# Kernel optimization log

Hardware: AMD Instinct MI355X
Metric: run time of the kernel (lower is better)

The kernel has to match this reference:

```python
import jax, jax.numpy as jnp
import numpy as np

CONFUSED_PAIRS = [(1, 2), (3, 4), (5, 6)]
NUM_CLASSES = 13
MARGIN = 0.5
IGNORE_INDEX = -100
BIG = 1e9  # finite sentinel instead of +/-inf (keeps grads clean)
EPS = 1e-12  # matches F.normalize eps

_conf_np = np.zeros((NUM_CLASSES, NUM_CLASSES), dtype=bool)
for _a, _b in CONFUSED_PAIRS:
    _conf_np[_a, _b] = True
    _conf_np[_b, _a] = True
CONF = jnp.asarray(_conf_np)  # [C, C] symmetric confused-class table


def setup_inputs() -> dict:
    key = jax.random.key(0)
    k1, k2 = jax.random.split(key)
    embeddings = jax.random.normal(k1, (16, 512, 256), dtype=jnp.float32)
    labels = jax.random.randint(k2, (16, 512), 0, 13, dtype=jnp.int64)
    return {"embeddings": embeddings, "labels": labels}


def reference(embeddings, labels):
    B, S, H = embeddings.shape
    e = embeddings.reshape(-1, H)                      # [N, H]
    lab = labels.reshape(-1)                           # [N]
    N = e.shape[0]

    valid = lab != IGNORE_INDEX                        # [N]
    # L2 normalize (F.normalize: divide by norm clamped to eps)
    norm = jnp.linalg.norm(e, axis=1, keepdims=True)
    e = e / jnp.maximum(norm, EPS)

    sim = e @ e.T                                      # [N, N] cosine sims

    lab_c = jnp.clip(lab, 0, NUM_CLASSES - 1)          # safe gather index
    # anchor label participates in some confused pair, and anchor is valid
    anchor_ok = valid & CONF[lab_c].any(axis=1)        # [N]

    same = lab[:, None] == lab[None, :]                # [N, N]
    eye = jnp.eye(N, dtype=bool)
    pos_mask = same & valid[None, :] & ~eye            # positives: same class, not self
    neg_mask = CONF[lab_c[:, None], lab_c[None, :]] & valid[None, :]  # confused-class negatives

    has_pos = pos_mask.any(axis=1)
    has_neg = neg_mask.any(axis=1)
    count_mask = anchor_ok & has_pos & has_neg         # [N] anchors contributing a triplet

    hardest_pos = jnp.min(jnp.where(pos_mask, sim, BIG), axis=1)   # [N]
    hardest_neg = jnp.max(jnp.where(neg_mask, sim, -BIG), axis=1)  # [N]

    triplet = jax.nn.relu(MARGIN + hardest_neg - hardest_pos)
    triplet = jnp.where(count_mask, triplet, 0.0)

    num_triplets = count_mask.sum()
    loss = triplet.sum() / jnp.maximum(num_triplets, 1).astype(triplet.dtype)
    return jnp.where(num_triplets > 0, loss, 0.0)
```

## Files before the change

kernel.cpp:

```cpp
#include <hip/hip_runtime.h>
#include <math.h>

#define Hdim    256
#define NMAX    8192
#define NCLS    13
#define NPADMAX (NMAX + 6 * 32)
#define WLMAX   264
#define NSPLIT  16
#define WPB     4
#define SIMGRID ((WLMAX * NSPLIT) / WPB)
#define BIGV    1e9f
#define MARGIN  0.5f

typedef __attribute__((ext_vector_type(8))) short bf16x8;
typedef __attribute__((ext_vector_type(4))) float f32x4;

struct WS {
    unsigned short ebf[NPADMAX][Hdim];
    unsigned hpK[NPADMAX];
    unsigned hnK[NPADMAX];
    int labG[NPADMAX];
    int gpos[NMAX];
    int S[8];
    int n[8];
    int wl_a[WLMAX];
    int wl_c[WLMAX];
    int T;
    unsigned done;
};

__device__ inline unsigned short f2bf(float f) {
    unsigned u = __float_as_uint(f);
    return (unsigned short)((u + 0x7fffu + ((u >> 16) & 1u)) >> 16);
}
__device__ inline unsigned fkey(float f) {
    unsigned u = __float_as_uint(f);
    return (u & 0x80000000u) ? ~u : (u | 0x80000000u);
}
__device__ inline float funkey(unsigned k) {
    unsigned u = (k & 0x80000000u) ? (k & 0x7fffffffu) : ~k;
    return __uint_as_float(u);
}

__global__ __launch_bounds__(1024) void plan_kernel(const int* __restrict__ lab,
                                                    WS* ws, int N) {
    __shared__ int h[8];
    __shared__ int S[8];
    __shared__ int cur[8];
    const int tid = threadIdx.x;
    if (tid < 8) h[tid] = 0;
    __syncthreads();
    for (int i = tid; i < N; i += 1024) {
        int l = lab[i];
        if (l >= 1 && l <= 6) atomicAdd(&h[l], 1);
    }
    __syncthreads();
    if (tid == 0) {
        int acc = 0;
        for (int c = 1; c <= 6; ++c) { S[c] = acc; acc += ((h[c] + 31) >> 5) << 5; }
        S[7] = acc;
        int T = 0;
        for (int c = 1; c <= 6; ++c) {
            int nt = (h[c] + 31) >> 5;
            for (int k = 0; k < nt; ++k) { ws->wl_a[T] = S[c] + 32 * k; ws->wl_c[T] = c; ++T; }
        }
        ws->T = T;
        ws->done = 0u;
        for (int c = 0; c < 8; ++c) { ws->n[c] = h[c]; ws->S[c] = S[c]; }
        ws->S[7] = S[7];
    }
    __syncthreads();
    const int SEnd = S[7];
    for (int g = tid; g < SEnd; g += 1024) {
        ws->hpK[g] = 0xFFFFFFFFu;
        ws->hnK[g] = 0u;
        ws->labG[g] = -1;
    }
    if (tid < 8) cur[tid] = S[tid];
    __syncthreads();
    for (int i = tid; i < N; i += 1024) {
        int l = lab[i];
        int g = -1;
        if (l >= 1 && l <= 6) { g = atomicAdd(&cur[l], 1); ws->labG[g] = l; }
        ws->gpos[i] = g;
    }
}

__global__ __launch_bounds__(1024) void norm_gather_kernel(const float* __restrict__ in,
                                                           WS* ws) {
    int row  = blockIdx.x * 16 + (threadIdx.x >> 6);
    int lane = threadIdx.x & 63;
    int g = ws->gpos[row];
    if (g < 0) return;
    float4 v = ((const float4*)(in + (size_t)row * Hdim))[lane];
    float ss = v.x*v.x + v.y*v.y + v.z*v.z + v.w*v.w;
    #pragma unroll
    for (int off = 32; off >= 1; off >>= 1) ss += __shfl_xor(ss, off);
    float sc = 1.0f / fmaxf(sqrtf(ss), 1e-12f);
    ushort4 o;
    o.x = f2bf(v.x * sc); o.y = f2bf(v.y * sc);
    o.z = f2bf(v.z * sc); o.w = f2bf(v.w * sc);
    ((ushort4*)(&ws->ebf[g][0]))[lane] = o;
}

__global__ __launch_bounds__(256) void sim_kernel(WS* ws, float* __restrict__ out) {
    const int wave = threadIdx.x >> 6;
    const int lane = threadIdx.x & 63;
    const int col  = lane & 15;
    const int quad = lane >> 4;
    const int wid  = blockIdx.x * WPB + wave;
    const int tileIdx = wid / NSPLIT;
    const int split   = wid % NSPLIT;

    if (tileIdx < ws->T) {
        const int aBase = ws->wl_a[tileIdx];
        const int c     = ws->wl_c[tileIdx];
        const int p     = ((c - 1) ^ 1) + 1;
        const int posS = ws->S[c], posRealE = posS + ws->n[c];
        const int negS = ws->S[p], negRealE = negS + ws->n[p];
        const int nPosT = (ws->S[c + 1] - posS) >> 4;
        const int nT    = nPosT + ((((p == c + 1) ? ws->S[p + 1] : ws->S[p])
                                    - negS) >> 4);
        const int nNegT = ((ws->S[p + 1]) - negS) >> 4;
        const int nTT = nPosT + nNegT;

        const unsigned short* ebf = &ws->ebf[0][0];

        bf16x8 afrag[2][8];
        #pragma unroll
        for (int t2 = 0; t2 < 2; ++t2) {
            const unsigned short* rp = ebf + (size_t)(aBase + t2 * 16 + col) * Hdim + quad * 8;
            #pragma unroll
            for (int ks = 0; ks < 8; ++ks)
                afrag[t2][ks] = *(const bf16x8*)(rp + ks * 32);
        }

        float runMin[2][4], runMax[2][4];
        #pragma unroll
        for (int t2 = 0; t2 < 2; ++t2)
            #pragma unroll
            for (int r = 0; r < 4; ++r) { runMin[t2][r] = BIGV; runMax[t2][r] = -BIGV; }

        auto j0Of = [&](int t) -> int {
            return (t < nPosT) ? (posS + (t << 4)) : (negS + ((t - nPosT) << 4));
        };
        bf16x8 b0[8], b1[8];
        auto loadB = [&](bf16x8 (&bf)[8], int t) {
            const unsigned short* rp = ebf + (size_t)(j0Of(t) + col) * Hdim + quad * 8;
            #pragma unroll
            for (int ks = 0; ks < 8; ++ks)
                bf[ks] = *(const bf16x8*)(rp + ks * 32);
        };
        auto computeT = [&](bf16x8 (&bf)[8], int t) {
            int j0 = j0Of(t);
            bool isPos = t < nPosT;
            int realE  = isPos ? posRealE : negRealE;
            bool valid = (j0 + col) < realE;
            #pragma unroll
            for (int t2 = 0; t2 < 2; ++t2) {
                f32x4 acc = {0.f, 0.f, 0.f, 0.f};
                #pragma unroll
                for (int ks = 0; ks < 8; ++ks)
                    acc = __builtin_amdgcn_mfma_f32_16x16x32_bf16(afrag[t2][ks], bf[ks], acc, 0, 0, 0);
                if (isPos) {
                    #pragma unroll
                    for (int r = 0; r < 4; ++r)
                        runMin[t2][r] = fminf(runMin[t2][r], valid ? acc[r] : BIGV);
                } else {
                    #pragma unroll
                    for (int r = 0; r < 4; ++r)
                        runMax[t2][r] = fmaxf(runMax[t2][r], valid ? acc[r] : -BIGV);
                }
            }
        };

        int nIter = (nTT > split) ? ((nTT - split + NSPLIT - 1) / NSPLIT) : 0;
        int t = split, i = 0;
        if (nIter > 0) loadB(b0, t);
        while (i + 2 <= nIter) {
            loadB(b1, t + NSPLIT);
            computeT(b0, t);
            if (i + 2 < nIter) loadB(b0, t + 2 * NSPLIT);
            computeT(b1, t + NSPLIT);
            t += 2 * NSPLIT; i += 2;
        }
        if (i < nIter) computeT(b0, t);
        (void)nT;

        #pragma unroll
        for (int t2 = 0; t2 < 2; ++t2)
            #pragma unroll
            for (int r = 0; r < 4; ++r) {
                float mn = runMin[t2][r], mx = runMax[t2][r];
                #pragma unroll
                for (int off = 1; off < 16; off <<= 1) {
                    mn = fminf(mn, __shfl_xor(mn, off));
                    mx = fmaxf(mx, __shfl_xor(mx, off));
                }
                if (col == 0) {
                    int a = aBase + t2 * 16 + quad * 4 + r;
                    if (mn < 1e8f)  atomicMin(&ws->hpK[a], fkey(mn));
                    if (mx > -1e8f) atomicMax(&ws->hnK[a], fkey(mx));
                }
            }
    }

    __shared__ int isLast;
    __syncthreads();
    if (threadIdx.x == 0) {
        __threadfence();
        unsigned old = atomicAdd(&ws->done, 1u);
        isLast = (old == (unsigned)(gridDim.x - 1)) ? 1 : 0;
    }
    __syncthreads();
    if (!isLast) return;
    __threadfence();

    __shared__ int ncls[8];
    if (threadIdx.x < 8) ncls[threadIdx.x] = ws->n[threadIdx.x];
    __syncthreads();
    float sum = 0.f; int cnt = 0;
    const int SEnd = ws->S[7];
    for (int g = threadIdx.x; g < SEnd; g += 256) {
        int l = ws->labG[g];
        if (l >= 1) {
            int p = ((l - 1) ^ 1) + 1;
            if (ncls[l] >= 2 && ncls[p] >= 1) {
                float hp = funkey(ws->hpK[g]);
                float hn = funkey(ws->hnK[g]);
                float tr = MARGIN + hn - hp;
                if (tr > 0.f) sum += tr;
                cnt += 1;
            }
        }
    }
    #pragma unroll
    for (int off = 32; off >= 1; off >>= 1) {
        sum += __shfl_xor(sum, off);
        cnt += __shfl_xor(cnt, off);
    }
    __shared__ float ssum[4]; __shared__ int scnt[4];
    int w = threadIdx.x >> 6;
    if ((threadIdx.x & 63) == 0) { ssum[w] = sum; scnt[w] = cnt; }
    __syncthreads();
    if (threadIdx.x == 0) {
        float ts = ssum[0] + ssum[1] + ssum[2] + ssum[3];
        int   tc = scnt[0] + scnt[1] + scnt[2] + scnt[3];
        out[0] = (tc > 0) ? ts / (float)tc : 0.f;
    }
}

extern "C" void kernel_launch(void* const* d_in, const int* in_sizes, int n_in,
                              void* d_out, int out_size, void* d_ws, size_t ws_size,
                              hipStream_t stream) {
    const float* emb = (const float*)d_in[0];
    const int*   lab = (const int*)d_in[1];
    int N = in_sizes[1];
    WS* ws = (WS*)d_ws;

    plan_kernel<<<1, 1024, 0, stream>>>(lab, ws, N);
    norm_gather_kernel<<<N / 16, 1024, 0, stream>>>(emb, ws);
    sim_kernel<<<SIMGRID, 256, 0, stream>>>(ws, (float*)d_out);
}
```

Measured before the change: 111.3 us.

## Assign one block per anchor tile and reduce loss in-block with atomics

Reworks the sim kernel so each block handles a full 32-anchor tile with its 4 waves splitting the column tiles. Hardest pos/neg are combined in LDS, and per-tile loss sums and counts go to global atomics, instead of per-anchor atomic min/max arrays and a last-block serial reduction. This removes the hp/hn/label initialization and the final pass over all anchors, and also shrinks norm_gather blocks. In exchange it launches far fewer waves, so each does more sequential MFMA work and GPU occupancy is lower.

```diff
diff --git a/kernel.cpp b/kernel.cpp
--- a/kernel.cpp
+++ b/kernel.cpp
@@ -3,12 +3,8 @@
 
 #define Hdim    256
 #define NMAX    8192
-#define NCLS    13
 #define NPADMAX (NMAX + 6 * 32)
 #define WLMAX   264
-#define NSPLIT  16
-#define WPB     4
-#define SIMGRID ((WLMAX * NSPLIT) / WPB)
 #define BIGV    1e9f
 #define MARGIN  0.5f
 
@@ -17,9 +13,6 @@
 
 struct WS {
     unsigned short ebf[NPADMAX][Hdim];
-    unsigned hpK[NPADMAX];
-    unsigned hnK[NPADMAX];
-    int labG[NPADMAX];
     int gpos[NMAX];
     int S[8];
     int n[8];
@@ -27,19 +20,13 @@
     int wl_c[WLMAX];
     int T;
     unsigned done;
+    float wsum;
+    int   wcnt;
 };
 
 __device__ inline unsigned short f2bf(float f) {
     unsigned u = __float_as_uint(f);
     return (unsigned short)((u + 0x7fffu + ((u >> 16) & 1u)) >> 16);
-}
-__device__ inline unsigned fkey(float f) {
-    unsigned u = __float_as_uint(f);
-    return (u & 0x80000000u) ? ~u : (u | 0x80000000u);
-}
-__device__ inline float funkey(unsigned k) {
-    unsigned u = (k & 0x80000000u) ? (k & 0x7fffffffu) : ~k;
-    return __uint_as_float(u);
 }
 
 __global__ __launch_bounds__(1024) void plan_kernel(const int* __restrict__ lab,
@@ -58,37 +45,28 @@
     if (tid == 0) {
         int acc = 0;
         for (int c = 1; c <= 6; ++c) { S[c] = acc; acc += ((h[c] + 31) >> 5) << 5; }
-        S[7] = acc;
+        S[0] = 0; S[7] = acc;
         int T = 0;
         for (int c = 1; c <= 6; ++c) {
             int nt = (h[c] + 31) >> 5;
             for (int k = 0; k < nt; ++k) { ws->wl_a[T] = S[c] + 32 * k; ws->wl_c[T] = c; ++T; }
         }
         ws->T = T;
-        ws->done = 0u;
+        ws->done = 0u; ws->wsum = 0.f; ws->wcnt = 0;
         for (int c = 0; c < 8; ++c) { ws->n[c] = h[c]; ws->S[c] = S[c]; }
-        ws->S[7] = S[7];
-    }
-    __syncthreads();
-    const int SEnd = S[7];
-    for (int g = tid; g < SEnd; g += 1024) {
-        ws->hpK[g] = 0xFFFFFFFFu;
-        ws->hnK[g] = 0u;
-        ws->labG[g] = -1;
-    }
+    }
+    __syncthreads();
     if (tid < 8) cur[tid] = S[tid];
     __syncthreads();
     for (int i = tid; i < N; i += 1024) {
         int l = lab[i];
-        int g = -1;
-        if (l >= 1 && l <= 6) { g = atomicAdd(&cur[l], 1); ws->labG[g] = l; }
-        ws->gpos[i] = g;
-    }
-}
-
-__global__ __launch_bounds__(1024) void norm_gather_kernel(const float* __restrict__ in,
-                                                           WS* ws) {
-    int row  = blockIdx.x * 16 + (threadIdx.x >> 6);
+        ws->gpos[i] = (l >= 1 && l <= 6) ? atomicAdd(&cur[l], 1) : -1;
+    }
+}
+
+__global__ __launch_bounds__(256) void norm_gather_kernel(const float* __restrict__ in,
+                                                          WS* ws) {
+    int row  = blockIdx.x * 4 + (threadIdx.x >> 6);
     int lane = threadIdx.x & 63;
     int g = ws->gpos[row];
     if (g < 0) return;
@@ -108,9 +86,9 @@
     const int lane = threadIdx.x & 63;
     const int col  = lane & 15;
     const int quad = lane >> 4;
-    const int wid  = blockIdx.x * WPB + wave;
-    const int tileIdx = wid / NSPLIT;
-    const int split   = wid % NSPLIT;
+    const int tileIdx = blockIdx.x;
+
+    __shared__ float lds_hp[4][32], lds_hn[4][32];
 
     if (tileIdx < ws->T) {
         const int aBase = ws->wl_a[tileIdx];
@@ -119,10 +97,9 @@
         const int posS = ws->S[c], posRealE = posS + ws->n[c];
         const int negS = ws->S[p], negRealE = negS + ws->n[p];
         const int nPosT = (ws->S[c + 1] - posS) >> 4;
-        const int nT    = nPosT + ((((p == c + 1) ? ws->S[p + 1] : ws->S[p])
-                                    - negS) >> 4);
-        const int nNegT = ((ws->S[p + 1]) - negS) >> 4;
-        const int nTT = nPosT + nNegT;
+        const int nNegT = (ws->S[p + 1] - negS) >> 4;
+        const int nTT   = nPosT + nNegT;
+        const bool hasPN = (ws->n[c] >= 2) && (ws->n[p] >= 1);
 
         const unsigned short* ebf = &ws->ebf[0][0];
 
@@ -174,18 +151,17 @@
             }
         };
 
-        int nIter = (nTT > split) ? ((nTT - split + NSPLIT - 1) / NSPLIT) : 0;
-        int t = split, i = 0;
+        int nIter = (nTT > wave) ? ((nTT - wave + 3) >> 2) : 0;
+        int t = wave, i = 0;
         if (nIter > 0) loadB(b0, t);
         while (i + 2 <= nIter) {
-            loadB(b1, t + NSPLIT);
+            loadB(b1, t + 4);
             computeT(b0, t);
-            if (i + 2 < nIter) loadB(b0, t + 2 * NSPLIT);
-            computeT(b1, t + NSPLIT);
-            t += 2 * NSPLIT; i += 2;
+            if (i + 2 < nIter) loadB(b0, t + 8);
+            computeT(b1, t + 4);
+            t += 8; i += 2;
         }
         if (i < nIter) computeT(b0, t);
-        (void)nT;
 
         #pragma unroll
         for (int t2 = 0; t2 < 2; ++t2)
@@ -198,55 +174,47 @@
                     mx = fmaxf(mx, __shfl_xor(mx, off));
                 }
                 if (col == 0) {
-                    int a = aBase + t2 * 16 + quad * 4 + r;
-                    if (mn < 1e8f)  atomicMin(&ws->hpK[a], fkey(mn));
-                    if (mx > -1e8f) atomicMax(&ws->hnK[a], fkey(mx));
-                }
-            }
-    }
-
-    __shared__ int isLast;
-    __syncthreads();
+                    int a = t2 * 16 + quad * 4 + r;
+                    lds_hp[wave][a] = mn;
+                    lds_hn[wave][a] = mx;
+                }
+            }
+        __syncthreads();
+
+        if (wave == 0) {
+            float contrib = 0.f; int cc = 0;
+            if (lane < 32) {
+                float hp = fminf(fminf(lds_hp[0][lane], lds_hp[1][lane]),
+                                 fminf(lds_hp[2][lane], lds_hp[3][lane]));
+                float hn = fmaxf(fmaxf(lds_hn[0][lane], lds_hn[1][lane]),
+                                 fmaxf(lds_hn[2][lane], lds_hn[3][lane]));
+                bool real = (aBase + lane) < posRealE;
+                if (real && hasPN) {
+                    float tr = MARGIN + hn - hp;
+                    contrib = (tr > 0.f) ? tr : 0.f;
+                    cc = 1;
+                }
+            }
+            #pragma unroll
+            for (int off = 32; off >= 1; off >>= 1) {
+                contrib += __shfl_xor(contrib, off);
+                cc      += __shfl_xor(cc, off);
+            }
+            if (lane == 0) {
+                atomicAdd(&ws->wsum, contrib);
+                atomicAdd(&ws->wcnt, cc);
+            }
+        }
+    }
+
     if (threadIdx.x == 0) {
-        __threadfence();
+        __builtin_amdgcn_s_waitcnt(0);
         unsigned old = atomicAdd(&ws->done, 1u);
-        isLast = (old == (unsigned)(gridDim.x - 1)) ? 1 : 0;
-    }
-    __syncthreads();
-    if (!isLast) return;
-    __threadfence();
-
-    __shared__ int ncls[8];
-    if (threadIdx.x < 8) ncls[threadIdx.x] = ws->n[threadIdx.x];
-    __syncthreads();
-    float sum = 0.f; int cnt = 0;
-    const int SEnd = ws->S[7];
-    for (int g = threadIdx.x; g < SEnd; g += 256) {
-        int l = ws->labG[g];
-        if (l >= 1) {
-            int p = ((l - 1) ^ 1) + 1;
-            if (ncls[l] >= 2 && ncls[p] >= 1) {
-                float hp = funkey(ws->hpK[g]);
-                float hn = funkey(ws->hnK[g]);
-                float tr = MARGIN + hn - hp;
-                if (tr > 0.f) sum += tr;
-                cnt += 1;
-            }
-        }
-    }
-    #pragma unroll
-    for (int off = 32; off >= 1; off >>= 1) {
-        sum += __shfl_xor(sum, off);
-        cnt += __shfl_xor(cnt, off);
-    }
-    __shared__ float ssum[4]; __shared__ int scnt[4];
-    int w = threadIdx.x >> 6;
-    if ((threadIdx.x & 63) == 0) { ssum[w] = sum; scnt[w] = cnt; }
-    __syncthreads();
-    if (threadIdx.x == 0) {
-        float ts = ssum[0] + ssum[1] + ssum[2] + ssum[3];
-        int   tc = scnt[0] + scnt[1] + scnt[2] + scnt[3];
-        out[0] = (tc > 0) ? ts / (float)tc : 0.f;
+        if (old == (unsigned)(gridDim.x - 1)) {
+            float s = atomicAdd(&ws->wsum, 0.0f);
+            int   n = atomicAdd(&ws->wcnt, 0);
+            out[0] = (n > 0) ? s / (float)n : 0.f;
+        }
     }
 }
 
@@ -259,6 +227,6 @@
     WS* ws = (WS*)d_ws;
 
     plan_kernel<<<1, 1024, 0, stream>>>(lab, ws, N);
-    norm_gather_kernel<<<N / 16, 1024, 0, stream>>>(emb, ws);
-    sim_kernel<<<SIMGRID, 256, 0, stream>>>(ws, (float*)d_out);
-}
+    norm_gather_kernel<<<(N + 3) / 4, 256, 0, stream>>>(emb, ws);
+    sim_kernel<<<WLMAX, 256, 0, stream>>>(ws, (float*)d_out);
+}
```

New measurement: 95.11 us, median of 2. 14.6% less time.

## Fuse plan and normalize kernels, use index indirection, persistent sim grid with LDS reduction

Applied to the files above, without the earlier changes.

Merges the label-planning and normalize kernels into one launch by normalizing every row in place and reaching class-grouped rows through an index array instead of a scatter that depended on the plan. The sim kernel becomes a persistent 256-block grid. Each block's four waves share one tile's column range, and their partial min/max results are combined in LDS before one global atomic per anchor. This saves a kernel launch and a dependency stage and cuts global atomics, at the cost of normalizing rows that are never used, an extra indirect load per fragment row, and per-tile block barriers.

```diff
diff --git a/kernel.cpp b/kernel.cpp
--- a/kernel.cpp
+++ b/kernel.cpp
@@ -3,12 +3,10 @@
 
 #define Hdim    256
 #define NMAX    8192
-#define NCLS    13
 #define NPADMAX (NMAX + 6 * 32)
 #define WLMAX   264
-#define NSPLIT  16
-#define WPB     4
-#define SIMGRID ((WLMAX * NSPLIT) / WPB)
+#define NSPLIT  2
+#define SIMGRID 256
 #define BIGV    1e9f
 #define MARGIN  0.5f
 
@@ -16,11 +14,11 @@
 typedef __attribute__((ext_vector_type(4))) float f32x4;
 
 struct WS {
-    unsigned short ebf[NPADMAX][Hdim];
+    unsigned short ebf[NMAX][Hdim];
+    int idx[NPADMAX];
+    int labG[NPADMAX];
     unsigned hpK[NPADMAX];
     unsigned hnK[NPADMAX];
-    int labG[NPADMAX];
-    int gpos[NMAX];
     int S[8];
     int n[8];
     int wl_a[WLMAX];
@@ -42,65 +40,64 @@
     return __uint_as_float(u);
 }
 
-__global__ __launch_bounds__(1024) void plan_kernel(const int* __restrict__ lab,
-                                                    WS* ws, int N) {
-    __shared__ int h[8];
-    __shared__ int S[8];
-    __shared__ int cur[8];
-    const int tid = threadIdx.x;
-    if (tid < 8) h[tid] = 0;
-    __syncthreads();
-    for (int i = tid; i < N; i += 1024) {
-        int l = lab[i];
-        if (l >= 1 && l <= 6) atomicAdd(&h[l], 1);
-    }
-    __syncthreads();
-    if (tid == 0) {
-        int acc = 0;
-        for (int c = 1; c <= 6; ++c) { S[c] = acc; acc += ((h[c] + 31) >> 5) << 5; }
-        S[7] = acc;
-        int T = 0;
-        for (int c = 1; c <= 6; ++c) {
-            int nt = (h[c] + 31) >> 5;
-            for (int k = 0; k < nt; ++k) { ws->wl_a[T] = S[c] + 32 * k; ws->wl_c[T] = c; ++T; }
-        }
-        ws->T = T;
-        ws->done = 0u;
-        for (int c = 0; c < 8; ++c) { ws->n[c] = h[c]; ws->S[c] = S[c]; }
-        ws->S[7] = S[7];
-    }
-    __syncthreads();
-    const int SEnd = S[7];
-    for (int g = tid; g < SEnd; g += 1024) {
-        ws->hpK[g] = 0xFFFFFFFFu;
-        ws->hnK[g] = 0u;
-        ws->labG[g] = -1;
-    }
-    if (tid < 8) cur[tid] = S[tid];
-    __syncthreads();
-    for (int i = tid; i < N; i += 1024) {
-        int l = lab[i];
-        int g = -1;
-        if (l >= 1 && l <= 6) { g = atomicAdd(&cur[l], 1); ws->labG[g] = l; }
-        ws->gpos[i] = g;
-    }
-}
-
-__global__ __launch_bounds__(1024) void norm_gather_kernel(const float* __restrict__ in,
-                                                           WS* ws) {
-    int row  = blockIdx.x * 16 + (threadIdx.x >> 6);
-    int lane = threadIdx.x & 63;
-    int g = ws->gpos[row];
-    if (g < 0) return;
-    float4 v = ((const float4*)(in + (size_t)row * Hdim))[lane];
-    float ss = v.x*v.x + v.y*v.y + v.z*v.z + v.w*v.w;
-    #pragma unroll
-    for (int off = 32; off >= 1; off >>= 1) ss += __shfl_xor(ss, off);
-    float sc = 1.0f / fmaxf(sqrtf(ss), 1e-12f);
-    ushort4 o;
-    o.x = f2bf(v.x * sc); o.y = f2bf(v.y * sc);
-    o.z = f2bf(v.z * sc); o.w = f2bf(v.w * sc);
-    ((ushort4*)(&ws->ebf[g][0]))[lane] = o;
+__global__ __launch_bounds__(256) void prep_kernel(const float* __restrict__ in,
+                                                   const int* __restrict__ lab,
+                                                   WS* ws, int N) {
+    const int b = blockIdx.x, tid = threadIdx.x;
+    if (b == 0) {
+        __shared__ int h[8], S[8], cur[8];
+        if (tid < 8) h[tid] = 0;
+        __syncthreads();
+        for (int i = tid; i < N; i += 256) {
+            int l = lab[i];
+            if (l >= 1 && l <= 6) atomicAdd(&h[l], 1);
+        }
+        __syncthreads();
+        if (tid == 0) {
+            int acc = 0; S[0] = 0;
+            for (int c = 1; c <= 6; ++c) { S[c] = acc; acc += ((h[c] + 31) >> 5) << 5; }
+            S[7] = acc;
+            int T = 0;
+            for (int c = 1; c <= 6; ++c) {
+                int nt = (h[c] + 31) >> 5;
+                for (int k = 0; k < nt; ++k) { ws->wl_a[T] = S[c] + 32 * k; ws->wl_c[T] = c; ++T; }
+            }
+            ws->T = T;
+            ws->done = 0u;
+            for (int c = 0; c < 8; ++c) { ws->n[c] = h[c]; ws->S[c] = S[c]; }
+        }
+        __syncthreads();
+        const int SEnd = S[7];
+        for (int g = tid; g < SEnd; g += 256) { ws->idx[g] = 0; ws->labG[g] = -1; }
+        if (tid < 8) cur[tid] = S[tid];
+        __syncthreads();
+        for (int i = tid; i < N; i += 256) {
+            int l = lab[i];
+            if (l >= 1 && l <= 6) { int g = atomicAdd(&cur[l], 1); ws->idx[g] = i; ws->labG[g] = l; }
+        }
+    } else {
+        const int wave = tid >> 6, lane = tid & 63;
+        const int r0 = (b - 1) * 16 + wave * 4;
+        #pragma unroll
+        for (int k = 0; k < 4; ++k) {
+            int row = r0 + k;
+            if (row < N) {
+                float4 v = ((const float4*)(in + (size_t)row * Hdim))[lane];
+                float ss = v.x*v.x + v.y*v.y + v.z*v.z + v.w*v.w;
+                #pragma unroll
+                for (int off = 32; off >= 1; off >>= 1) ss += __shfl_xor(ss, off);
+                float sc = 1.0f / fmaxf(sqrtf(ss), 1e-12f);
+                ushort4 o;
+                o.x = f2bf(v.x * sc); o.y = f2bf(v.y * sc);
+                o.z = f2bf(v.z * sc); o.w = f2bf(v.w * sc);
+                ((ushort4*)(&ws->ebf[row][0]))[lane] = o;
+            }
+        }
+        if (tid < 17) {
+            int g = (b - 1) * 17 + tid;
+            if (g < NPADMAX) { ws->hpK[g] = 0xFFFFFFFFu; ws->hnK[g] = 0u; }
+        }
+    }
 }
 
 __global__ __launch_bounds__(256) void sim_kernel(WS* ws, float* __restrict__ out) {
@@ -108,28 +105,29 @@
     const int lane = threadIdx.x & 63;
     const int col  = lane & 15;
     const int quad = lane >> 4;
-    const int wid  = blockIdx.x * WPB + wave;
-    const int tileIdx = wid / NSPLIT;
-    const int split   = wid % NSPLIT;
-
-    if (tileIdx < ws->T) {
+    const int T    = ws->T;
+
+    __shared__ float lds_hp[4][32], lds_hn[4][32];
+
+    for (int w = blockIdx.x; w < T * NSPLIT; w += gridDim.x) {
+        const int tileIdx = w >> 1, split = w & 1;
         const int aBase = ws->wl_a[tileIdx];
         const int c     = ws->wl_c[tileIdx];
         const int p     = ((c - 1) ^ 1) + 1;
         const int posS = ws->S[c], posRealE = posS + ws->n[c];
         const int negS = ws->S[p], negRealE = negS + ws->n[p];
         const int nPosT = (ws->S[c + 1] - posS) >> 4;
-        const int nT    = nPosT + ((((p == c + 1) ? ws->S[p + 1] : ws->S[p])
-                                    - negS) >> 4);
-        const int nNegT = ((ws->S[p + 1]) - negS) >> 4;
-        const int nTT = nPosT + nNegT;
+        const int nNegT = (ws->S[p + 1] - negS) >> 4;
+        const int nTT   = nPosT + nNegT;
 
         const unsigned short* ebf = &ws->ebf[0][0];
+        const int* __restrict__ idx = ws->idx;
 
         bf16x8 afrag[2][8];
         #pragma unroll
         for (int t2 = 0; t2 < 2; ++t2) {
-            const unsigned short* rp = ebf + (size_t)(aBase + t2 * 16 + col) * Hdim + quad * 8;
+            int row = idx[aBase + t2 * 16 + col];
+            const unsigned short* rp = ebf + (size_t)row * Hdim + quad * 8;
             #pragma unroll
             for (int ks = 0; ks < 8; ++ks)
                 afrag[t2][ks] = *(const bf16x8*)(rp + ks * 32);
@@ -146,7 +144,8 @@
         };
         bf16x8 b0[8], b1[8];
         auto loadB = [&](bf16x8 (&bf)[8], int t) {
-            const unsigned short* rp = ebf + (size_t)(j0Of(t) + col) * Hdim + quad * 8;
+            int row = idx[j0Of(t) + col];
+            const unsigned short* rp = ebf + (size_t)row * Hdim + quad * 8;
             #pragma unroll
             for (int ks = 0; ks < 8; ++ks)
                 bf[ks] = *(const bf16x8*)(rp + ks * 32);
@@ -174,18 +173,18 @@
             }
         };
 
-        int nIter = (nTT > split) ? ((nTT - split + NSPLIT - 1) / NSPLIT) : 0;
-        int t = split, i = 0;
+        const int first = split + NSPLIT * wave;
+        int nIter = (nTT > first) ? ((nTT - first + 7) >> 3) : 0;
+        int t = first, i = 0;
         if (nIter > 0) loadB(b0, t);
         while (i + 2 <= nIter) {
-            loadB(b1, t + NSPLIT);
+            loadB(b1, t + 8);
             computeT(b0, t);
-            if (i + 2 < nIter) loadB(b0, t + 2 * NSPLIT);
-            computeT(b1, t + NSPLIT);
-            t += 2 * NSPLIT; i += 2;
+            if (i + 2 < nIter) loadB(b0, t + 16);
+            computeT(b1, t + 8);
+            t += 16; i += 2;
         }
         if (i < nIter) computeT(b0, t);
-        (void)nT;
 
         #pragma unroll
         for (int t2 = 0; t2 < 2; ++t2)
@@ -198,22 +197,31 @@
                     mx = fmaxf(mx, __shfl_xor(mx, off));
                 }
                 if (col == 0) {
-                    int a = aBase + t2 * 16 + quad * 4 + r;
-                    if (mn < 1e8f)  atomicMin(&ws->hpK[a], fkey(mn));
-                    if (mx > -1e8f) atomicMax(&ws->hnK[a], fkey(mx));
+                    int a = t2 * 16 + quad * 4 + r;
+                    lds_hp[wave][a] = mn;
+                    lds_hn[wave][a] = mx;
                 }
             }
-    }
-
-    __shared__ int isLast;
+        __syncthreads();
+        if (wave == 0 && lane < 32) {
+            float hp = fminf(fminf(lds_hp[0][lane], lds_hp[1][lane]),
+                             fminf(lds_hp[2][lane], lds_hp[3][lane]));
+            float hn = fmaxf(fmaxf(lds_hn[0][lane], lds_hn[1][lane]),
+                             fmaxf(lds_hn[2][lane], lds_hn[3][lane]));
+            int a = aBase + lane;
+            if (hp < 1e8f)  atomicMin(&ws->hpK[a], fkey(hp));
+            if (hn > -1e8f) atomicMax(&ws->hnK[a], fkey(hn));
+        }
+        __syncthreads();
+    }
+
+    __shared__ unsigned oldv;
+    if (threadIdx.x == 0) {
+        __builtin_amdgcn_s_waitcnt(0);
+        oldv = atomicAdd(&ws->done, 1u);
+    }
     __syncthreads();
-    if (threadIdx.x == 0) {
-        __threadfence();
-        unsigned old = atomicAdd(&ws->done, 1u);
-        isLast = (old == (unsigned)(gridDim.x - 1)) ? 1 : 0;
-    }
-    __syncthreads();
-    if (!isLast) return;
+    if (oldv != (unsigned)(gridDim.x - 1)) return;
     __threadfence();
 
     __shared__ int ncls[8];
@@ -240,8 +248,7 @@
         cnt += __shfl_xor(cnt, off);
     }
     __shared__ float ssum[4]; __shared__ int scnt[4];
-    int w = threadIdx.x >> 6;
-    if ((threadIdx.x & 63) == 0) { ssum[w] = sum; scnt[w] = cnt; }
+    if ((threadIdx.x & 63) == 0) { ssum[threadIdx.x >> 6] = sum; scnt[threadIdx.x >> 6] = cnt; }
     __syncthreads();
     if (threadIdx.x == 0) {
         float ts = ssum[0] + ssum[1] + ssum[2] + ssum[3];
@@ -258,7 +265,6 @@
     int N = in_sizes[1];
     WS* ws = (WS*)d_ws;
 
-    plan_kernel<<<1, 1024, 0, stream>>>(lab, ws, N);
-    norm_gather_kernel<<<N / 16, 1024, 0, stream>>>(emb, ws);
+    prep_kernel<<<1 + (N + 15) / 16, 256, 0, stream>>>(emb, lab, ws, N);
     sim_kernel<<<SIMGRID, 256, 0, stream>>>(ws, (float*)d_out);
 }
```

Measured after the change: 109.3 us. No clear change (-1.8%).
